# Kernel optimization log

Hardware: AMD Instinct MI355X
Metric: run time of the kernel (lower is better)

Reference implementation:

```python
import jax, jax.numpy as jnp
import numpy as np


def setup_inputs() -> dict:
    key = jax.random.key(0)
    k1, k2 = jax.random.split(key)
    n, d, num_classes = 262144, 128, 512
    inputs = jax.random.normal(k1, (n, d), dtype=jnp.float32)
    targets = jax.random.randint(k2, (n,), 0, num_classes)
    return {"inputs": inputs, "targets": targets, "num_classes": num_classes}


def reference(inputs, targets, num_classes):
    beta = 0.1
    eps = 1e-12  # torch F.normalize default eps (norm clamped to min eps)
    # L2-normalize features
    x = inputs / jnp.maximum(jnp.linalg.norm(inputs, axis=1, keepdims=True), eps)  # [n, d]

    # Per-class centers: mean of normalized features, then L2-normalize, detached.
    ones = jnp.ones((x.shape[0],), dtype=x.dtype)
    counts = jax.ops.segment_sum(ones, targets, num_segments=num_classes)          # [C]
    csum = jax.ops.segment_sum(x, targets, num_segments=num_classes)               # [C, d]
    cmean = csum / jnp.maximum(counts, 1.0)[:, None]
    centers = cmean / jnp.maximum(jnp.linalg.norm(cmean, axis=1, keepdims=True), eps)
    centers = jax.lax.stop_gradient(centers)  # .detach() in original

    # Numerator logit: center of own class dotted with own feature
    pos = jnp.sum(centers[targets] * x, axis=1) / beta                             # [n]
    # Denominator: sum of exp over all *present* classes (original only builds
    # centers for pids that appear in the batch)
    scores = jnp.exp(centers @ x.T / beta)                                         # [C, n]
    present = counts > 0
    denom = jnp.sum(jnp.where(present[:, None], scores, 0.0), axis=0)              # [n]
    return -jnp.mean(pos - jnp.log(denom))
```

## Files before the change

kernel.cpp:

```cpp
#include <hip/hip_runtime.h>
#include <stdint.h>

#define NROWS 262144
#define DDIM 128
#define NCLS 512
#define NHB 64
constexpr float INV_BETA = 10.0f;
constexpr float EXP2_SCALE = 14.426950408889634f;

typedef __bf16 v8bf __attribute__((ext_vector_type(8)));
typedef float v4f __attribute__((ext_vector_type(4)));

__device__ inline unsigned short f2bf(float f) {
    uint32_t u = __builtin_bit_cast(uint32_t, f);
    u += 0x7FFFu + ((u >> 16) & 1u);
    return (unsigned short)(u >> 16);
}
__device__ inline float bflo(uint32_t u) { return __builtin_bit_cast(float, u << 16); }
__device__ inline float bfhi(uint32_t u) { return __builtin_bit_cast(float, u & 0xFFFF0000u); }

#define GLL16(gsrc, ldst)                                                        \
    __builtin_amdgcn_global_load_lds(                                            \
        (const __attribute__((address_space(1))) void*)(uintptr_t)(gsrc),        \
        (__attribute__((address_space(3))) void*)(uintptr_t)(ldst), 16, 0, 0)

__global__ __launch_bounds__(256) void k1_normalize(
    const float* __restrict__ in, const int* __restrict__ tgt,
    unsigned short* __restrict__ xb, int* __restrict__ bh) {
    __shared__ int h[NCLS];
    int t = threadIdx.x;
    if (blockIdx.x >= 8192) {
        int b = blockIdx.x - 8192;
        for (int i = t; i < NCLS; i += 256) h[i] = 0;
        __syncthreads();
        int base = b * (NROWS / NHB);
        for (int i = base + t; i < base + NROWS / NHB; i += 256)
            atomicAdd(&h[tgt[i]], 1);
        __syncthreads();
        for (int i = t; i < NCLS; i += 256)
            bh[b * NCLS + i] = h[i];
        return;
    }
    int w = t >> 6;
    int half = (t & 63) >> 5;
    int lane32 = t & 31;
    int hw = blockIdx.x * 8 + w * 2 + half;
    int r0 = hw * 4;
    float4 v[4];
#pragma unroll
    for (int j = 0; j < 4; ++j)
        v[j] = *reinterpret_cast<const float4*>(in + (size_t)(r0 + j) * DDIM + lane32 * 4);
    float s[4];
#pragma unroll
    for (int j = 0; j < 4; ++j)
        s[j] = v[j].x * v[j].x + v[j].y * v[j].y + v[j].z * v[j].z + v[j].w * v[j].w;
#pragma unroll
    for (int off = 1; off < 32; off <<= 1) {
#pragma unroll
        for (int j = 0; j < 4; ++j) s[j] += __shfl_xor(s[j], off);
    }
#pragma unroll
    for (int j = 0; j < 4; ++j) {
        float iv = rsqrtf(fmaxf(s[j], 1e-24f));
        ushort4 o;
        o.x = f2bf(v[j].x * iv); o.y = f2bf(v[j].y * iv);
        o.z = f2bf(v[j].z * iv); o.w = f2bf(v[j].w * iv);
        *reinterpret_cast<ushort4*>(xb + (size_t)(r0 + j) * DDIM + lane32 * 4) = o;
    }
}

__global__ __launch_bounds__(512) void k_prefix(
    const int* __restrict__ bh, int* __restrict__ counts, int* __restrict__ offs,
    int* __restrict__ base, float* __restrict__ nabsG, float* __restrict__ out) {
    __shared__ int sc[NCLS];
    __shared__ int za;
    int t = threadIdx.x;
    int cnt = 0;
#pragma unroll 8
    for (int b = 0; b < NHB; ++b) cnt += bh[b * NCLS + t];
    counts[t] = cnt;
    sc[t] = cnt;
    if (t == 0) za = 0;
    __syncthreads();
    for (int off = 1; off < NCLS; off <<= 1) {
        int v = (t >= off) ? sc[t - off] : 0;
        __syncthreads();
        sc[t] += v;
        __syncthreads();
    }
    int excl = sc[t] - cnt;
    offs[t] = excl;
    if (cnt == 0) atomicAdd(&za, 1);
    int run = excl;
    for (int b = 0; b < NHB; ++b) {
        base[b * NCLS + t] = run;
        run += bh[b * NCLS + t];
    }
    __syncthreads();
    if (t == 0) { *nabsG = (float)za; *out = 0.0f; }
}

__global__ __launch_bounds__(256) void k_scatter(
    const int* __restrict__ tgt, const int* __restrict__ base, int* __restrict__ ridx) {
    __shared__ int cur[NCLS];
    int t = threadIdx.x;
    int b = blockIdx.x;
    cur[t] = base[b * NCLS + t];
    cur[t + 256] = base[b * NCLS + t + 256];
    __syncthreads();
    int r0 = b * (NROWS / NHB);
    for (int i = t; i < NROWS / NHB; i += 256) {
        int row = r0 + i;
        int c = tgt[row];
        int pos = atomicAdd(&cur[c], 1);
        ridx[pos] = row;
    }
}

__global__ __launch_bounds__(512) void k_centers(
    const unsigned short* __restrict__ xb, const int* __restrict__ ridx,
    const int* __restrict__ counts, const int* __restrict__ offs,
    unsigned short* __restrict__ cen, float* __restrict__ out) {
    __shared__ float2 sP[8][64];
    int t = threadIdx.x, w = t >> 6, l = t & 63;
    int cl = blockIdx.x;
    int cnt = counts[cl], start = offs[cl];
    const uint32_t* xb32 = (const uint32_t*)xb;
    float a0 = 0.0f, a1 = 0.0f;
    int per = (cnt + 7) >> 3;
    int lo = w * per, hi = min(cnt, lo + per);
    int i = lo;
    for (; i + 8 <= hi; i += 8) {
        int id[8]; uint32_t v[8];
#pragma unroll
        for (int j = 0; j < 8; ++j) id[j] = ridx[start + i + j];
#pragma unroll
        for (int j = 0; j < 8; ++j) v[j] = xb32[(size_t)id[j] * 64 + l];
#pragma unroll
        for (int j = 0; j < 8; ++j) { a0 += bflo(v[j]); a1 += bfhi(v[j]); }
    }
    for (; i < hi; ++i) {
        uint32_t v = xb32[(size_t)ridx[start + i] * 64 + l];
        a0 += bflo(v); a1 += bfhi(v);
    }
    sP[w][l] = make_float2(a0, a1);
    __syncthreads();
    if (w == 0) {
        float c0 = 0.0f, c1 = 0.0f;
#pragma unroll
        for (int q = 0; q < 8; ++q) { c0 += sP[q][l].x; c1 += sP[q][l].y; }
        float fc = fmaxf((float)cnt, 1.0f);
        c0 /= fc; c1 /= fc;
        float ss = c0 * c0 + c1 * c1;
        for (int off = 1; off < 64; off <<= 1) ss += __shfl_xor(ss, off);
        float inv = EXP2_SCALE / fmaxf(sqrtf(ss), 1e-12f);
        ushort2 o;
        o.x = f2bf(c0 * inv); o.y = f2bf(c1 * inv);
        *reinterpret_cast<ushort2*>(cen + (size_t)cl * DDIM + l * 2) = o;
        if (l == 0)
            atomicAdd(out, -(float)cnt * sqrtf(ss) * (INV_BETA / (float)NROWS));
    }
}

__global__ __launch_bounds__(1024) void k4_loss(
    const unsigned short* __restrict__ xb, const unsigned short* __restrict__ cen,
    const float* __restrict__ nabsG, float* __restrict__ out) {
    extern __shared__ char lds[];
    char* xL0 = lds;
    char* xL1 = lds + 32768;
    float* denP = (float*)(lds + 65536);
    float* wsum = (float*)(lds + 81920);
    int t = threadIdx.x, w = t >> 6, l = t & 63;
    int lm = l & 15, lk = l >> 4;
    float nabs = *nabsG;

    v8bf afr[2][4];
#pragma unroll
    for (int m = 0; m < 2; ++m)
#pragma unroll
        for (int kc = 0; kc < 4; ++kc) {
            int arow = w * 32 + m * 16 + lm;
            afr[m][kc] = *reinterpret_cast<const v8bf*>(cen + (size_t)arow * DDIM + kc * 32 + lk * 8);
        }

    int block0 = blockIdx.x * 1024;
    const char* xbB = (const char*)xb + (size_t)block0 * 256;

    int C0 = w * 128 + l;
    int C1 = C0 + 64;
    int so0 = (C0 >> 4) * 256 + ((((C0 & 15) ^ ((C0 >> 4) & 7))) << 4);
    int so1 = (C1 >> 4) * 256 + ((((C1 & 15) ^ ((C1 >> 4) & 7))) << 4);
    int dw = w * 2048;

    GLL16(xbB + so0, xL0 + dw);
    GLL16(xbB + so1, xL0 + dw + 1024);
    float lossAcc = 0.0f;
    int rs = w * 8 + (l >> 3);
    int rq = (l & 7) * 2;
    asm volatile("s_waitcnt vmcnt(0)" ::: "memory");
    __syncthreads();

    for (int tile = 0; tile < 8; ++tile) {
        char* xc = (tile & 1) ? xL1 : xL0;
        char* xn = (tile & 1) ? xL0 : xL1;
        float* dp = denP + (tile & 1) * 2048;
        if (tile < 7) {
            const char* s = xbB + (size_t)(tile + 1) * 32768;
            GLL16(s + so0, xn + dw);
            GLL16(s + so1, xn + dw + 1024);
        }

#pragma unroll
        for (int h = 0; h < 2; ++h) {
            v4f acc[2][4];
            v4f zero = {0.0f, 0.0f, 0.0f, 0.0f};
#pragma unroll
            for (int m = 0; m < 2; ++m)
#pragma unroll
                for (int n = 0; n < 4; ++n) acc[m][n] = zero;

#pragma unroll
            for (int kc = 0; kc < 4; ++kc) {
                int kb = kc * 64 + lk * 16;
                v8bf b[4];
#pragma unroll
                for (int n = 0; n < 4; ++n) {
                    int brow = h * 64 + n * 16 + lm;
                    b[n] = *reinterpret_cast<const v8bf*>(xc + brow * 256 + (kb ^ ((brow & 7) << 4)));
                }
#pragma unroll
                for (int m = 0; m < 2; ++m)
#pragma unroll
                    for (int n = 0; n < 4; ++n)
                        acc[m][n] = __builtin_amdgcn_mfma_f32_16x16x32_bf16(afr[m][kc], b[n], acc[m][n], 0, 0, 0);
            }

#pragma unroll
            for (int n = 0; n < 4; ++n) {
                float se = 0.0f;
#pragma unroll
                for (int m = 0; m < 2; ++m) {
#pragma unroll
                    for (int rr = 0; rr < 4; ++rr)
                        se += __builtin_amdgcn_exp2f(acc[m][n][rr]);
                }
                se += __shfl_xor(se, 16); se += __shfl_xor(se, 32);
                if (l < 16) dp[w * 128 + h * 64 + n * 16 + lm] = se;
            }
        }
        asm volatile("s_waitcnt vmcnt(0)" ::: "memory");
        __syncthreads();
        float den = dp[rq * 128 + rs] + dp[(rq + 1) * 128 + rs];
        den += __shfl_xor(den, 1);
        den += __shfl_xor(den, 2);
        den += __shfl_xor(den, 4);
        if ((l & 7) == 0) lossAcc += __logf(den - nabs);
    }
    lossAcc += __shfl_xor(lossAcc, 8);
    lossAcc += __shfl_xor(lossAcc, 16);
    lossAcc += __shfl_xor(lossAcc, 32);
    if (l == 0) wsum[w] = lossAcc;
    __syncthreads();
    if (t == 0) {
        float s = 0.0f;
#pragma unroll
        for (int q = 0; q < 16; ++q) s += wsum[q];
        atomicAdd(out, s * (1.0f / NROWS));
    }
}

extern "C" void kernel_launch(void* const* d_in, const int* in_sizes, int n_in,
                              void* d_out, int out_size, void* d_ws, size_t ws_size,
                              hipStream_t stream) {
    const float* in = (const float*)d_in[0];
    const int* tgt = (const int*)d_in[1];
    float* out = (float*)d_out;
    char* ws = (char*)d_ws;
    unsigned short* xb = (unsigned short*)(ws);
    int* counts = (int*)(ws + 67108864);
    int* offs = (int*)(ws + 67110912);
    float* nabsG = (float*)(ws + 67112960);
    unsigned short* cen = (unsigned short*)(ws + 67115264);
    int* ridx = (int*)(ws + 67246336);
    int* bh = (int*)(ws + 68294912);
    int* base = (int*)(ws + 68557056);

    (void)hipFuncSetAttribute((const void*)k4_loss,
                              hipFuncAttributeMaxDynamicSharedMemorySize, 81984);

    hipLaunchKernelGGL(k1_normalize, dim3(8192 + NHB), dim3(256), 0, stream, in, tgt, xb, bh);
    hipLaunchKernelGGL(k_prefix, dim3(1), dim3(512), 0, stream, bh, counts, offs, base, nabsG, out);
    hipLaunchKernelGGL(k_scatter, dim3(NHB), dim3(256), 0, stream, tgt, base, ridx);
    hipLaunchKernelGGL(k_centers, dim3(NCLS), dim3(512), 0, stream, xb, ridx, counts, offs, cen, out);
    hipLaunchKernelGGL(k4_loss, dim3(256), dim3(1024), 81984, stream, xb, cen, nabsG, out);
}
```

Baseline: 111.4 us.

## Stage all centers in LDS and keep feature fragments in registers

The loss kernel is restructured so each block loads all 512 class centers into LDS once (swizzled) while each wave holds its 64 feature rows as MFMA B fragments in registers. It then loops over the 32 center tiles and accumulates exp2 sums per row in registers. This removes the double-buffered feature tiles, the per-tile LDS partial-denominator exchange and the block barriers in the main loop. The cost is 128KB of LDS per block, which limits occupancy to one block per CU, plus repeated LDS reads of the center fragments. The center gather loop is also unrolled from 8 to 16 loads to put more loads in flight.

```diff
diff --git a/kernel.cpp b/kernel.cpp
--- a/kernel.cpp
+++ b/kernel.cpp
@@ -117,6 +117,25 @@
     }
 }
 
+__device__ inline void centers_gather(
+    const uint32_t* __restrict__ xb32, const int* __restrict__ ridx,
+    int start, int lo, int hi, int l, float& a0, float& a1) {
+    int i = lo;
+    for (; i + 16 <= hi; i += 16) {
+        int id[16]; uint32_t v[16];
+#pragma unroll
+        for (int j = 0; j < 16; ++j) id[j] = ridx[start + i + j];
+#pragma unroll
+        for (int j = 0; j < 16; ++j) v[j] = xb32[(size_t)id[j] * 64 + l];
+#pragma unroll
+        for (int j = 0; j < 16; ++j) { a0 += bflo(v[j]); a1 += bfhi(v[j]); }
+    }
+    for (; i < hi; ++i) {
+        uint32_t v = xb32[(size_t)ridx[start + i] * 64 + l];
+        a0 += bflo(v); a1 += bfhi(v);
+    }
+}
+
 __global__ __launch_bounds__(512) void k_centers(
     const unsigned short* __restrict__ xb, const int* __restrict__ ridx,
     const int* __restrict__ counts, const int* __restrict__ offs,
@@ -125,24 +144,10 @@
     int t = threadIdx.x, w = t >> 6, l = t & 63;
     int cl = blockIdx.x;
     int cnt = counts[cl], start = offs[cl];
-    const uint32_t* xb32 = (const uint32_t*)xb;
     float a0 = 0.0f, a1 = 0.0f;
     int per = (cnt + 7) >> 3;
     int lo = w * per, hi = min(cnt, lo + per);
-    int i = lo;
-    for (; i + 8 <= hi; i += 8) {
-        int id[8]; uint32_t v[8];
-#pragma unroll
-        for (int j = 0; j < 8; ++j) id[j] = ridx[start + i + j];
-#pragma unroll
-        for (int j = 0; j < 8; ++j) v[j] = xb32[(size_t)id[j] * 64 + l];
-#pragma unroll
-        for (int j = 0; j < 8; ++j) { a0 += bflo(v[j]); a1 += bfhi(v[j]); }
-    }
-    for (; i < hi; ++i) {
-        uint32_t v = xb32[(size_t)ridx[start + i] * 64 + l];
-        a0 += bflo(v); a1 += bfhi(v);
-    }
+    centers_gather((const uint32_t*)xb, ridx, start, lo, hi, l, a0, a1);
     sP[w][l] = make_float2(a0, a1);
     __syncthreads();
     if (w == 0) {
@@ -166,99 +171,67 @@
     const unsigned short* __restrict__ xb, const unsigned short* __restrict__ cen,
     const float* __restrict__ nabsG, float* __restrict__ out) {
     extern __shared__ char lds[];
-    char* xL0 = lds;
-    char* xL1 = lds + 32768;
-    float* denP = (float*)(lds + 65536);
-    float* wsum = (float*)(lds + 81920);
+    char* cenL = lds;
+    float* wsum = (float*)(lds + 131072);
     int t = threadIdx.x, w = t >> 6, l = t & 63;
     int lm = l & 15, lk = l >> 4;
     float nabs = *nabsG;
 
-    v8bf afr[2][4];
-#pragma unroll
-    for (int m = 0; m < 2; ++m)
+    int s0 = blockIdx.x * 1024 + w * 64;
+    const char* xB = (const char*)xb;
+    v8bf bfr[4][4];
+#pragma unroll
+    for (int n = 0; n < 4; ++n)
+#pragma unroll
+        for (int kc = 0; kc < 4; ++kc)
+            bfr[n][kc] = *reinterpret_cast<const v8bf*>(
+                xB + (size_t)(s0 + n * 16 + lm) * 256 + kc * 64 + lk * 16);
+
+    const char* cB = (const char*)cen;
+#pragma unroll
+    for (int i = 0; i < 8; ++i) {
+        int C = w * 512 + i * 64 + l;
+        int src = (C >> 4) * 256 + ((((C & 15) ^ ((C >> 4) & 7))) << 4);
+        GLL16(cB + src, cenL + w * 8192 + i * 1024);
+    }
+    asm volatile("s_waitcnt vmcnt(0)" ::: "memory");
+    __syncthreads();
+
+    float den[4] = {0.0f, 0.0f, 0.0f, 0.0f};
+    for (int m = 0; m < 32; ++m) {
+        v8bf a[4];
 #pragma unroll
         for (int kc = 0; kc < 4; ++kc) {
-            int arow = w * 32 + m * 16 + lm;
-            afr[m][kc] = *reinterpret_cast<const v8bf*>(cen + (size_t)arow * DDIM + kc * 32 + lk * 8);
+            int row = m * 16 + lm;
+            a[kc] = *reinterpret_cast<const v8bf*>(
+                cenL + row * 256 + ((kc * 64 + lk * 16) ^ ((row & 7) << 4)));
         }
-
-    int block0 = blockIdx.x * 1024;
-    const char* xbB = (const char*)xb + (size_t)block0 * 256;
-
-    int C0 = w * 128 + l;
-    int C1 = C0 + 64;
-    int so0 = (C0 >> 4) * 256 + ((((C0 & 15) ^ ((C0 >> 4) & 7))) << 4);
-    int so1 = (C1 >> 4) * 256 + ((((C1 & 15) ^ ((C1 >> 4) & 7))) << 4);
-    int dw = w * 2048;
-
-    GLL16(xbB + so0, xL0 + dw);
-    GLL16(xbB + so1, xL0 + dw + 1024);
+        v4f acc[4];
+        v4f zero = {0.0f, 0.0f, 0.0f, 0.0f};
+#pragma unroll
+        for (int n = 0; n < 4; ++n) acc[n] = zero;
+#pragma unroll
+        for (int kc = 0; kc < 4; ++kc)
+#pragma unroll
+            for (int n = 0; n < 4; ++n)
+                acc[n] = __builtin_amdgcn_mfma_f32_16x16x32_bf16(a[kc], bfr[n][kc], acc[n], 0, 0, 0);
+#pragma unroll
+        for (int n = 0; n < 4; ++n)
+#pragma unroll
+            for (int rr = 0; rr < 4; ++rr)
+                den[n] += __builtin_amdgcn_exp2f(acc[n][rr]);
+    }
+
     float lossAcc = 0.0f;
-    int rs = w * 8 + (l >> 3);
-    int rq = (l & 7) * 2;
-    asm volatile("s_waitcnt vmcnt(0)" ::: "memory");
-    __syncthreads();
-
-    for (int tile = 0; tile < 8; ++tile) {
-        char* xc = (tile & 1) ? xL1 : xL0;
-        char* xn = (tile & 1) ? xL0 : xL1;
-        float* dp = denP + (tile & 1) * 2048;
-        if (tile < 7) {
-            const char* s = xbB + (size_t)(tile + 1) * 32768;
-            GLL16(s + so0, xn + dw);
-            GLL16(s + so1, xn + dw + 1024);
-        }
-
-#pragma unroll
-        for (int h = 0; h < 2; ++h) {
-            v4f acc[2][4];
-            v4f zero = {0.0f, 0.0f, 0.0f, 0.0f};
-#pragma unroll
-            for (int m = 0; m < 2; ++m)
-#pragma unroll
-                for (int n = 0; n < 4; ++n) acc[m][n] = zero;
-
-#pragma unroll
-            for (int kc = 0; kc < 4; ++kc) {
-                int kb = kc * 64 + lk * 16;
-                v8bf b[4];
-#pragma unroll
-                for (int n = 0; n < 4; ++n) {
-                    int brow = h * 64 + n * 16 + lm;
-                    b[n] = *reinterpret_cast<const v8bf*>(xc + brow * 256 + (kb ^ ((brow & 7) << 4)));
-                }
-#pragma unroll
-                for (int m = 0; m < 2; ++m)
-#pragma unroll
-                    for (int n = 0; n < 4; ++n)
-                        acc[m][n] = __builtin_amdgcn_mfma_f32_16x16x32_bf16(afr[m][kc], b[n], acc[m][n], 0, 0, 0);
-            }
-
-#pragma unroll
-            for (int n = 0; n < 4; ++n) {
-                float se = 0.0f;
-#pragma unroll
-                for (int m = 0; m < 2; ++m) {
-#pragma unroll
-                    for (int rr = 0; rr < 4; ++rr)
-                        se += __builtin_amdgcn_exp2f(acc[m][n][rr]);
-                }
-                se += __shfl_xor(se, 16); se += __shfl_xor(se, 32);
-                if (l < 16) dp[w * 128 + h * 64 + n * 16 + lm] = se;
-            }
-        }
-        asm volatile("s_waitcnt vmcnt(0)" ::: "memory");
-        __syncthreads();
-        float den = dp[rq * 128 + rs] + dp[(rq + 1) * 128 + rs];
-        den += __shfl_xor(den, 1);
-        den += __shfl_xor(den, 2);
-        den += __shfl_xor(den, 4);
-        if ((l & 7) == 0) lossAcc += __logf(den - nabs);
-    }
-    lossAcc += __shfl_xor(lossAcc, 8);
-    lossAcc += __shfl_xor(lossAcc, 16);
-    lossAcc += __shfl_xor(lossAcc, 32);
+#pragma unroll
+    for (int n = 0; n < 4; ++n) {
+        float d = den[n];
+        d += __shfl_xor(d, 16);
+        d += __shfl_xor(d, 32);
+        if (l < 16) lossAcc += __logf(d - nabs);
+    }
+#pragma unroll
+    for (int off = 1; off < 64; off <<= 1) lossAcc += __shfl_xor(lossAcc, off);
     if (l == 0) wsum[w] = lossAcc;
     __syncthreads();
     if (t == 0) {
@@ -286,11 +259,11 @@
     int* base = (int*)(ws + 68557056);
 
     (void)hipFuncSetAttribute((const void*)k4_loss,
-                              hipFuncAttributeMaxDynamicSharedMemorySize, 81984);
+                              hipFuncAttributeMaxDynamicSharedMemorySize, 131136);
 
     hipLaunchKernelGGL(k1_normalize, dim3(8192 + NHB), dim3(256), 0, stream, in, tgt, xb, bh);
     hipLaunchKernelGGL(k_prefix, dim3(1), dim3(512), 0, stream, bh, counts, offs, base, nabsG, out);
     hipLaunchKernelGGL(k_scatter, dim3(NHB), dim3(256), 0, stream, tgt, base, ridx);
     hipLaunchKernelGGL(k_centers, dim3(NCLS), dim3(512), 0, stream, xb, ridx, counts, offs, cen, out);
-    hipLaunchKernelGGL(k4_loss, dim3(256), dim3(1024), 81984, stream, xb, cen, nabsG, out);
-}
+    hipLaunchKernelGGL(k4_loss, dim3(256), dim3(1024), 131136, stream, xb, cen, nabsG, out);
+}
```

Measured after the change: 108.8 us. 1.02x faster.
